# Optimization experiments

Measured on AMD Instinct MI355X. Metric: run time of the kernel, lower is better.

Reference implementation:

```python
import jax, jax.numpy as jnp
import numpy as np

BATCH = 1024


def setup_inputs() -> dict:
    key = jax.random.key(0)
    ks = jax.random.split(key, 8)
    piece_positions = jax.random.randint(ks[0], (BATCH, 64, 10), 0, 2) > 0  # bool occupancy
    king_positions = jax.random.randint(ks[1], (BATCH, 2), 0, 64, dtype=jnp.int32)
    input_weights = jax.random.randint(ks[2], (64, 641, 256), -32768, 32767, dtype=jnp.int16)
    input_bias = jnp.zeros((256,), dtype=jnp.int16)
    w1 = jax.random.randint(ks[3], (32, 512), -128, 127, dtype=jnp.int8)
    b1 = jnp.zeros((32,), dtype=jnp.int32)
    w2 = jax.random.randint(ks[4], (32, 32), -128, 127, dtype=jnp.int8)
    b2 = jnp.zeros((32,), dtype=jnp.int32)
    out_w = jax.random.randint(ks[5], (32,), -128, 127, dtype=jnp.int8)
    out_b = jnp.zeros((1,), dtype=jnp.int32)
    return {
        'piece_positions': piece_positions, 'king_positions': king_positions,
        'input_weights': input_weights, 'input_bias': input_bias,
        'w1': w1, 'b1': b1, 'w2': w2, 'b2': b2, 'out_w': out_w, 'out_b': out_b,
    }


def _fc(x, w, b):
    # int8 inputs/weights, int32 accumulate, floor-div 64, clamp to [0,127] -> int8
    y = x.astype(jnp.int32) @ w.T.astype(jnp.int32) + b
    y = jnp.floor_divide(y, 64)
    return jnp.clip(y, 0, 127).astype(jnp.int8)


def reference(piece_positions, king_positions, input_weights, input_bias,
              w1, b1, w2, b2, out_w, out_b):
    B = piece_positions.shape[0]
    pp = piece_positions.reshape(B, 640).astype(jnp.int32)  # flattened 64x10 HalfKP features

    def half(king_idx):
        wk = input_weights[king_idx]            # (B, 641, 256) gathered per-sample king table
        feats = wk[:, :640, :].astype(jnp.int32)
        kbias = wk[:, 640, :].astype(jnp.int32)
        return jnp.einsum('bf,bfd->bd', pp, feats) + kbias  # (B, 256)

    white = half(king_positions[:, 0])
    black = half(king_positions[:, 1])
    # int16 wraparound semantics of the original: accumulate in int32, mod-cast to int16
    acc = (white + black + input_bias.astype(jnp.int32)).astype(jnp.int16)

    x = jnp.clip(acc, 0, 127).astype(jnp.int8)
    x = jnp.concatenate([x, x], axis=1)  # (B, 512) side_to_move || other_side
    x = _fc(x, w1, b1)
    x = _fc(x, w2, b2)
    s = jnp.sum(x.astype(jnp.int32) * out_w.astype(jnp.int32)) + out_b  # scalar sum over batch too (as in source)
    return jnp.floor_divide(s, 16)  # shape (1,)
```

## Files before the change

### kernel.cpp

```cpp
#include <hip/hip_runtime.h>
#include <stdint.h>

#define NDIM  256
#define NFEAT 640
#define NROWS 641

struct SharedBuf {
    uint8_t pp[NFEAT];
    int     acc[4][NDIM];
    alignas(16) int8_t x[NDIM];
    int     fc[256];
    alignas(4) int8_t x2[32];
    int     list[4][160];
};

__global__ void detect_layout(const int* __restrict__ W32, const int* __restrict__ pp32,
                              int* __restrict__ ws) {
    int raww = 0, rawpp = 0;
    for (int i = 0; i < 16; ++i) {
        const int v = W32[i];
        if (v > 32767 || v < -32768) raww = 1;
        const int u = pp32[i];
        if (u != 0 && u != 1) rawpp = 1;
    }
    ws[0] = 0;
    ws[1] = raww;
    ws[2] = rawpp;
}

template<bool RAWW, bool RAWPP>
__device__ __forceinline__ void nnue_body(
    const void* __restrict__ ppv, const int* __restrict__ kp,
    const void* __restrict__ Wv,  const void* __restrict__ ibv,
    const void* __restrict__ w1v, const int* __restrict__ b1,
    const void* __restrict__ w2v, const int* __restrict__ b2,
    const void* __restrict__ owv, int* __restrict__ ws, SharedBuf& sh)
{
    const int b = blockIdx.x;
    const int t = threadIdx.x;
    const int l = t & 63;
    const int g = t >> 6;

    if (RAWPP) {
        const uint32_t* src = (const uint32_t*)((const uint8_t*)ppv + (size_t)b * NFEAT);
        if (t < NFEAT / 4) ((uint32_t*)sh.pp)[t] = src[t];
    } else {
        const int* src = (const int*)ppv + (size_t)b * NFEAT;
        for (int i = t; i < NFEAT; i += 256) sh.pp[i] = (uint8_t)(src[i] != 0);
    }
    __syncthreads();

    const int base = g * 160;
    int cnt = 0;
    for (int c = 0; c < 160; c += 64) {
        const int idx = c + l;
        const bool flag = (idx < 160) && (sh.pp[base + idx] != 0);
        const unsigned long long m = __ballot(flag);
        const int pos = cnt + (int)__popcll(m & ((1ull << l) - 1ull));
        if (flag) sh.list[g][pos] = base + idx;
        cnt += (int)__popcll(m);
    }

    const int k0 = kp[b * 2 + 0];
    const int k1 = kp[b * 2 + 1];

    int a0 = 0, a1 = 0, a2 = 0, a3 = 0, a4 = 0, a5 = 0, a6 = 0, a7 = 0;

    if (RAWW) {
        const char* W0 = (const char*)Wv + (size_t)k0 * (NROWS * NDIM * 2);
        const char* W1 = (const char*)Wv + (size_t)k1 * (NROWS * NDIM * 2);
        const int lo = l * 8;
        auto step = [&](int f) {
            const uint2 u0 = *(const uint2*)(W0 + f * 512 + lo);
            const uint2 u1 = *(const uint2*)(W1 + f * 512 + lo);
            a0 += (int)(u0.x & 0xFFFFu); a1 += (int)(u0.x >> 16);
            a2 += (int)(u0.y & 0xFFFFu); a3 += (int)(u0.y >> 16);
            a4 += (int)(u1.x & 0xFFFFu); a5 += (int)(u1.x >> 16);
            a6 += (int)(u1.y & 0xFFFFu); a7 += (int)(u1.y >> 16);
        };
        int j = 0;
        for (; j + 4 <= cnt; j += 4) {
            const int f0 = sh.list[g][j], f1 = sh.list[g][j + 1];
            const int f2 = sh.list[g][j + 2], f3 = sh.list[g][j + 3];
            step(f0); step(f1); step(f2); step(f3);
        }
        for (; j < cnt; ++j) step(sh.list[g][j]);
    } else {
        const char* W0 = (const char*)Wv + (size_t)k0 * (NROWS * NDIM * 4);
        const char* W1 = (const char*)Wv + (size_t)k1 * (NROWS * NDIM * 4);
        const int lo = l * 16;
        auto step = [&](int f) {
            const int4 u0 = *(const int4*)(W0 + f * 1024 + lo);
            const int4 u1 = *(const int4*)(W1 + f * 1024 + lo);
            a0 += u0.x; a1 += u0.y; a2 += u0.z; a3 += u0.w;
            a4 += u1.x; a5 += u1.y; a6 += u1.z; a7 += u1.w;
        };
        int j = 0;
        for (; j + 4 <= cnt; j += 4) {
            const int f0 = sh.list[g][j], f1 = sh.list[g][j + 1];
            const int f2 = sh.list[g][j + 2], f3 = sh.list[g][j + 3];
            step(f0); step(f1); step(f2); step(f3);
        }
        for (; j < cnt; ++j) step(sh.list[g][j]);
    }

    sh.acc[g][4 * l + 0] = a0 + a4;
    sh.acc[g][4 * l + 1] = a1 + a5;
    sh.acc[g][4 * l + 2] = a2 + a6;
    sh.acc[g][4 * l + 3] = a3 + a7;
    __syncthreads();

    {
        const int d = t;
        int tot = sh.acc[0][d] + sh.acc[1][d] + sh.acc[2][d] + sh.acc[3][d];
        int kb0, kb1, ibx;
        if (RAWW) {
            const int16_t* Wq = (const int16_t*)Wv;
            kb0 = Wq[((size_t)k0 * NROWS + NFEAT) * NDIM + d];
            kb1 = Wq[((size_t)k1 * NROWS + NFEAT) * NDIM + d];
            ibx = ((const int16_t*)ibv)[d];
        } else {
            const int* Wq = (const int*)Wv;
            kb0 = Wq[((size_t)k0 * NROWS + NFEAT) * NDIM + d];
            kb1 = Wq[((size_t)k1 * NROWS + NFEAT) * NDIM + d];
            ibx = ((const int*)ibv)[d];
        }
        tot += kb0 + kb1 + ibx;
        int v = (int)(int16_t)(uint16_t)(uint32_t)tot;
        v = v < 0 ? 0 : (v > 127 ? 127 : v);
        sh.x[d] = (int8_t)v;
    }
    __syncthreads();

    {
        const int o = t >> 3, part = t & 7;
        int y = 0;
        const uint32_t* xw = (const uint32_t*)sh.x;
        if (RAWW) {
            const uint32_t* w1r = (const uint32_t*)((const char*)w1v + o * 512);
            #pragma unroll
            for (int i = 0; i < 8; ++i) {
                const int wi = part * 8 + i;
                const uint32_t xv = xw[wi];
                const uint32_t wa = w1r[wi];
                const uint32_t wb = w1r[64 + wi];
                #pragma unroll
                for (int jj = 0; jj < 4; ++jj) {
                    const int xj  = (int)((xv >> (8 * jj)) & 0xFFu);
                    const int waj = (int)(int8_t)(uint8_t)(wa >> (8 * jj));
                    const int wbj = (int)(int8_t)(uint8_t)(wb >> (8 * jj));
                    y += xj * (waj + wbj);
                }
            }
        } else {
            const int* w1r = (const int*)w1v + o * 512;
            #pragma unroll
            for (int i = 0; i < 8; ++i) {
                const int wi = part * 8 + i;
                const uint32_t xv = xw[wi];
                #pragma unroll
                for (int jj = 0; jj < 4; ++jj) {
                    const int xj = (int)((xv >> (8 * jj)) & 0xFFu);
                    y += xj * (w1r[wi * 4 + jj] + w1r[256 + wi * 4 + jj]);
                }
            }
        }
        sh.fc[t] = y;
    }
    __syncthreads();

    if (t < 32) {
        int y = b1[t];
        #pragma unroll
        for (int p = 0; p < 8; ++p) y += sh.fc[t * 8 + p];
        y >>= 6;
        y = y < 0 ? 0 : (y > 127 ? 127 : y);
        sh.x2[t] = (int8_t)y;
    }
    __syncthreads();

    if (t < 32) {
        int y = b2[t];
        const uint32_t* x2w = (const uint32_t*)sh.x2;
        if (RAWW) {
            const uint32_t* w2r = (const uint32_t*)((const char*)w2v + t * 32);
            #pragma unroll
            for (int i = 0; i < 8; ++i) {
                const uint32_t xv = x2w[i];
                const uint32_t wv = w2r[i];
                #pragma unroll
                for (int jj = 0; jj < 4; ++jj)
                    y += (int)((xv >> (8 * jj)) & 0xFFu) * (int)(int8_t)(uint8_t)(wv >> (8 * jj));
            }
        } else {
            const int* w2r = (const int*)w2v + t * 32;
            #pragma unroll
            for (int i = 0; i < 8; ++i) {
                const uint32_t xv = x2w[i];
                #pragma unroll
                for (int jj = 0; jj < 4; ++jj)
                    y += (int)((xv >> (8 * jj)) & 0xFFu) * w2r[i * 4 + jj];
            }
        }
        y >>= 6;
        y = y < 0 ? 0 : (y > 127 ? 127 : y);
        const int owx = RAWW ? (int)((const int8_t*)owv)[t] : ((const int*)owv)[t];
        int p = y * owx;
        #pragma unroll
        for (int off = 16; off > 0; off >>= 1) p += __shfl_down(p, off, 32);
        if (t == 0) atomicAdd(ws, p);
    }
}

__global__ __launch_bounds__(256, 4) void nnue_main(
    const void* __restrict__ pp, const int* __restrict__ kp,
    const void* __restrict__ W,  const void* __restrict__ ib,
    const void* __restrict__ w1, const int* __restrict__ b1,
    const void* __restrict__ w2, const int* __restrict__ b2,
    const void* __restrict__ ow, int* __restrict__ ws)
{
    __shared__ SharedBuf sh;
    const int raww = ws[1], rawpp = ws[2];
    if (raww) {
        if (rawpp) nnue_body<true,  true >(pp, kp, W, ib, w1, b1, w2, b2, ow, ws, sh);
        else       nnue_body<true,  false>(pp, kp, W, ib, w1, b1, w2, b2, ow, ws, sh);
    } else {
        if (rawpp) nnue_body<false, true >(pp, kp, W, ib, w1, b1, w2, b2, ow, ws, sh);
        else       nnue_body<false, false>(pp, kp, W, ib, w1, b1, w2, b2, ow, ws, sh);
    }
}

__global__ void nnue_finalize(const int* __restrict__ ws, const int* __restrict__ ob,
                              int* __restrict__ out) {
    out[0] = (ws[0] + ob[0]) >> 4;
}

extern "C" void kernel_launch(void* const* d_in, const int* in_sizes, int n_in,
                              void* d_out, int out_size, void* d_ws, size_t ws_size,
                              hipStream_t stream)
{
    const void* pp = d_in[0];
    const int*  kp = (const int*)d_in[1];
    const void* W  = d_in[2];
    const void* ib = d_in[3];
    const void* w1 = d_in[4];
    const int*  b1 = (const int*)d_in[5];
    const void* w2 = d_in[6];
    const int*  b2 = (const int*)d_in[7];
    const void* ow = d_in[8];
    const int*  ob = (const int*)d_in[9];
    int* ws  = (int*)d_ws;
    int* out = (int*)d_out;

    const int B = in_sizes[1] / 2;

    hipLaunchKernelGGL(detect_layout, dim3(1), dim3(1), 0, stream,
                       (const int*)W, (const int*)pp, ws);
    hipLaunchKernelGGL(nnue_main, dim3(B), dim3(256), 0, stream,
                       pp, kp, W, ib, w1, b1, w2, b2, ow, ws);
    hipLaunchKernelGGL(nnue_finalize, dim3(1), dim3(1), 0, stream, ws, ob, out);
}
```

Measured before the change: 172.0 us.

## Bucket samples by king square and gather weights once per king bucket

Adds a bucketing kernel that sorts the 2B king slots by king index, then a gather kernel where each block handles one king (split into 8 parts) and streams that king's weight table once, accumulating up to 8 samples at a time via per-feature bitmasks. A combine kernel then sums the two halves per sample and runs the small FC layers. This reuses each king's weight rows across many samples instead of re-reading them per sample. In exchange it adds two kernel launches, a single-block serial bucketing pass, a workspace partial buffer, and dense row scans instead of sparse feature lists. The old monolithic path is kept as a fallback when the workspace is too small.

```diff
diff --git a/kernel.cpp b/kernel.cpp
--- a/kernel.cpp
+++ b/kernel.cpp
@@ -4,6 +4,268 @@
 #define NDIM  256
 #define NFEAT 640
 #define NROWS 641
+#define SG    8
+#define PARTS 8
+
+__global__ void nnue_bucket(const int* __restrict__ kp, const int* __restrict__ W32,
+                            const int* __restrict__ pp32, int nslots,
+                            int* __restrict__ ws,
+                            int* __restrict__ king_start, int* __restrict__ slot_list,
+                            int* __restrict__ slot_pos)
+{
+    __shared__ int cnt[64];
+    __shared__ int off[64];
+    const int t = threadIdx.x;
+    if (t < 64) cnt[t] = 0;
+    if (t == 0) {
+        int raww = 0, rawpp = 0;
+        for (int i = 0; i < 16; ++i) {
+            const int v = W32[i];
+            if (v > 32767 || v < -32768) raww = 1;
+            const int u = pp32[i];
+            if (u != 0 && u != 1) rawpp = 1;
+        }
+        ws[0] = 0; ws[1] = raww; ws[2] = rawpp;
+    }
+    __syncthreads();
+    for (int s = t; s < nslots; s += 256) atomicAdd(&cnt[kp[s]], 1);
+    __syncthreads();
+    if (t == 0) {
+        int run = 0;
+        for (int k = 0; k < 64; ++k) { off[k] = run; king_start[k] = run; run += cnt[k]; }
+        king_start[64] = run;
+    }
+    __syncthreads();
+    for (int s = t; s < nslots; s += 256) {
+        const int k = kp[s];
+        const int pos = atomicAdd(&off[k], 1);
+        slot_list[pos] = s;
+        slot_pos[s] = pos;
+    }
+}
+
+struct GatherLds {
+    int samp[SG];
+    unsigned mask[NFEAT];
+    int acci[4][SG][NDIM];
+};
+
+template<bool RAWW, bool RAWPP>
+__device__ __forceinline__ void gather_body(
+    const void* __restrict__ ppv, const void* __restrict__ Wv,
+    const int* __restrict__ king_start, const int* __restrict__ slot_list,
+    int* __restrict__ partial, GatherLds& sh)
+{
+    const int bid = blockIdx.x;
+    const int k = bid & 63;
+    const int p = bid >> 6;
+    const int t = threadIdx.x, l = t & 63, g = t >> 6;
+
+    const int s0 = king_start[k], s1 = king_start[k + 1];
+    const int m = s1 - s0;
+    const int chunk = (m + PARTS - 1) / PARTS;
+    const int lo = s0 + p * chunk;
+    const int hi = min(lo + chunk, s1);
+    if (lo >= hi) return;
+
+    const char* Wk = (const char*)Wv + (size_t)k * NROWS * NDIM * (RAWW ? 2 : 4);
+    int kb;
+    if (RAWW) kb = (int)*(const int16_t*)(Wk + ((size_t)NFEAT * NDIM + t) * 2);
+    else      kb = *(const int*)(Wk + ((size_t)NFEAT * NDIM + t) * 4);
+
+    for (int base = lo; base < hi; base += SG) {
+        const int ns = min(SG, hi - base);
+        if (t < ns) sh.samp[t] = slot_list[base + t] >> 1;
+        __syncthreads();
+
+        for (int r = t; r < NFEAT; r += 256) {
+            unsigned mm = 0;
+            for (int i = 0; i < ns; ++i) {
+                const int s = sh.samp[i];
+                int v;
+                if (RAWPP) v = ((const uint8_t*)ppv)[(size_t)s * NFEAT + r];
+                else       v = ((const int*)ppv)[(size_t)s * NFEAT + r];
+                mm |= (v != 0 ? 1u : 0u) << i;
+            }
+            sh.mask[r] = mm;
+        }
+        __syncthreads();
+
+        int4 acc[SG];
+        #pragma unroll
+        for (int i = 0; i < SG; ++i) acc[i] = make_int4(0, 0, 0, 0);
+
+        const int rbeg = g * (NFEAT / 4), rend = rbeg + (NFEAT / 4);
+        #pragma unroll 2
+        for (int r = rbeg; r < rend; ++r) {
+            unsigned mm = sh.mask[r];
+            mm = __builtin_amdgcn_readfirstlane(mm);
+            int v0, v1, v2, v3;
+            if (RAWW) {
+                const uint2 u = *(const uint2*)(Wk + (size_t)r * 512 + l * 8);
+                v0 = (int)(u.x & 0xFFFFu); v1 = (int)(u.x >> 16);
+                v2 = (int)(u.y & 0xFFFFu); v3 = (int)(u.y >> 16);
+            } else {
+                const int4 u = *(const int4*)(Wk + (size_t)r * 1024 + l * 16);
+                v0 = u.x; v1 = u.y; v2 = u.z; v3 = u.w;
+            }
+            #pragma unroll
+            for (int i = 0; i < SG; ++i)
+                if (mm & (1u << i)) { acc[i].x += v0; acc[i].y += v1; acc[i].z += v2; acc[i].w += v3; }
+        }
+
+        #pragma unroll
+        for (int i = 0; i < SG; ++i) ((int4*)&sh.acci[g][i][0])[l] = acc[i];
+        __syncthreads();
+        for (int i = 0; i < ns; ++i) {
+            const int sum = sh.acci[0][i][t] + sh.acci[1][i][t]
+                          + sh.acci[2][i][t] + sh.acci[3][i][t] + kb;
+            partial[(size_t)(base + i) * NDIM + t] = sum;
+        }
+        __syncthreads();
+    }
+}
+
+__global__ __launch_bounds__(256, 2) void nnue_gather(
+    const void* __restrict__ pp, const void* __restrict__ W,
+    const int* __restrict__ ws, const int* __restrict__ king_start,
+    const int* __restrict__ slot_list, int* __restrict__ partial)
+{
+    __shared__ GatherLds sh;
+    const int raww = ws[1], rawpp = ws[2];
+    if (raww) {
+        if (rawpp) gather_body<true,  true >(pp, W, king_start, slot_list, partial, sh);
+        else       gather_body<true,  false>(pp, W, king_start, slot_list, partial, sh);
+    } else {
+        if (rawpp) gather_body<false, true >(pp, W, king_start, slot_list, partial, sh);
+        else       gather_body<false, false>(pp, W, king_start, slot_list, partial, sh);
+    }
+}
+
+struct CombineLds {
+    alignas(16) int8_t x[NDIM];
+    int fc[256];
+    alignas(4) int8_t x2[32];
+};
+
+template<bool RAWW>
+__device__ __forceinline__ void combine_body(
+    const int* __restrict__ partial, const int* __restrict__ slot_pos,
+    const void* __restrict__ ibv,
+    const void* __restrict__ w1v, const int* __restrict__ b1,
+    const void* __restrict__ w2v, const int* __restrict__ b2,
+    const void* __restrict__ owv, int* __restrict__ ws, CombineLds& sh)
+{
+    const int b = blockIdx.x;
+    const int t = threadIdx.x;
+
+    const int i0 = slot_pos[2 * b + 0];
+    const int i1 = slot_pos[2 * b + 1];
+    {
+        int tot = partial[(size_t)i0 * NDIM + t] + partial[(size_t)i1 * NDIM + t];
+        tot += RAWW ? (int)((const int16_t*)ibv)[t] : ((const int*)ibv)[t];
+        int v = (int)(int16_t)(uint16_t)(uint32_t)tot;
+        v = v < 0 ? 0 : (v > 127 ? 127 : v);
+        sh.x[t] = (int8_t)v;
+    }
+    __syncthreads();
+
+    {
+        const int o = t >> 3, part = t & 7;
+        int y = 0;
+        const uint32_t* xw = (const uint32_t*)sh.x;
+        if (RAWW) {
+            const uint32_t* w1r = (const uint32_t*)((const char*)w1v + o * 512);
+            #pragma unroll
+            for (int i = 0; i < 8; ++i) {
+                const int wi = part * 8 + i;
+                const uint32_t xv = xw[wi];
+                const uint32_t wa = w1r[wi];
+                const uint32_t wb = w1r[64 + wi];
+                #pragma unroll
+                for (int jj = 0; jj < 4; ++jj) {
+                    const int xj  = (int)((xv >> (8 * jj)) & 0xFFu);
+                    const int waj = (int)(int8_t)(uint8_t)(wa >> (8 * jj));
+                    const int wbj = (int)(int8_t)(uint8_t)(wb >> (8 * jj));
+                    y += xj * (waj + wbj);
+                }
+            }
+        } else {
+            const int* w1r = (const int*)w1v + o * 512;
+            #pragma unroll
+            for (int i = 0; i < 8; ++i) {
+                const int wi = part * 8 + i;
+                const uint32_t xv = xw[wi];
+                #pragma unroll
+                for (int jj = 0; jj < 4; ++jj) {
+                    const int xj = (int)((xv >> (8 * jj)) & 0xFFu);
+                    y += xj * (w1r[wi * 4 + jj] + w1r[256 + wi * 4 + jj]);
+                }
+            }
+        }
+        sh.fc[t] = y;
+    }
+    __syncthreads();
+
+    if (t < 32) {
+        int y = b1[t];
+        #pragma unroll
+        for (int p = 0; p < 8; ++p) y += sh.fc[t * 8 + p];
+        y >>= 6;
+        y = y < 0 ? 0 : (y > 127 ? 127 : y);
+        sh.x2[t] = (int8_t)y;
+    }
+    __syncthreads();
+
+    if (t < 32) {
+        int y = b2[t];
+        const uint32_t* x2w = (const uint32_t*)sh.x2;
+        if (RAWW) {
+            const uint32_t* w2r = (const uint32_t*)((const char*)w2v + t * 32);
+            #pragma unroll
+            for (int i = 0; i < 8; ++i) {
+                const uint32_t xv = x2w[i];
+                const uint32_t wv = w2r[i];
+                #pragma unroll
+                for (int jj = 0; jj < 4; ++jj)
+                    y += (int)((xv >> (8 * jj)) & 0xFFu) * (int)(int8_t)(uint8_t)(wv >> (8 * jj));
+            }
+        } else {
+            const int* w2r = (const int*)w2v + t * 32;
+            #pragma unroll
+            for (int i = 0; i < 8; ++i) {
+                const uint32_t xv = x2w[i];
+                #pragma unroll
+                for (int jj = 0; jj < 4; ++jj)
+                    y += (int)((xv >> (8 * jj)) & 0xFFu) * w2r[i * 4 + jj];
+            }
+        }
+        y >>= 6;
+        y = y < 0 ? 0 : (y > 127 ? 127 : y);
+        const int owx = RAWW ? (int)((const int8_t*)owv)[t] : ((const int*)owv)[t];
+        int pr = y * owx;
+        #pragma unroll
+        for (int off = 16; off > 0; off >>= 1) pr += __shfl_down(pr, off, 32);
+        if (t == 0) atomicAdd(ws, pr);
+    }
+}
+
+__global__ __launch_bounds__(256) void nnue_combine(
+    const int* __restrict__ partial, const int* __restrict__ slot_pos,
+    const void* __restrict__ ib,
+    const void* __restrict__ w1, const int* __restrict__ b1,
+    const void* __restrict__ w2, const int* __restrict__ b2,
+    const void* __restrict__ ow, int* __restrict__ ws)
+{
+    __shared__ CombineLds sh;
+    if (ws[1]) combine_body<true >(partial, slot_pos, ib, w1, b1, w2, b2, ow, ws, sh);
+    else       combine_body<false>(partial, slot_pos, ib, w1, b1, w2, b2, ow, ws, sh);
+}
+
+__global__ void nnue_finalize(const int* __restrict__ ws, const int* __restrict__ ob,
+                              int* __restrict__ out) {
+    out[0] = (ws[0] + ob[0]) >> 4;
+}
 
 struct SharedBuf {
     uint8_t pp[NFEAT];
@@ -23,13 +285,11 @@
         const int u = pp32[i];
         if (u != 0 && u != 1) rawpp = 1;
     }
-    ws[0] = 0;
-    ws[1] = raww;
-    ws[2] = rawpp;
+    ws[0] = 0; ws[1] = raww; ws[2] = rawpp;
 }
 
 template<bool RAWW, bool RAWPP>
-__device__ __forceinline__ void nnue_body(
+__device__ __forceinline__ void mono_body(
     const void* __restrict__ ppv, const int* __restrict__ kp,
     const void* __restrict__ Wv,  const void* __restrict__ ibv,
     const void* __restrict__ w1v, const int* __restrict__ b1,
@@ -55,15 +315,14 @@
     for (int c = 0; c < 160; c += 64) {
         const int idx = c + l;
         const bool flag = (idx < 160) && (sh.pp[base + idx] != 0);
-        const unsigned long long m = __ballot(flag);
-        const int pos = cnt + (int)__popcll(m & ((1ull << l) - 1ull));
+        const unsigned long long mmask = __ballot(flag);
+        const int pos = cnt + (int)__popcll(mmask & ((1ull << l) - 1ull));
         if (flag) sh.list[g][pos] = base + idx;
-        cnt += (int)__popcll(m);
+        cnt += (int)__popcll(mmask);
     }
 
     const int k0 = kp[b * 2 + 0];
     const int k1 = kp[b * 2 + 1];
-
     int a0 = 0, a1 = 0, a2 = 0, a3 = 0, a4 = 0, a5 = 0, a6 = 0, a7 = 0;
 
     if (RAWW) {
@@ -205,14 +464,14 @@
         y >>= 6;
         y = y < 0 ? 0 : (y > 127 ? 127 : y);
         const int owx = RAWW ? (int)((const int8_t*)owv)[t] : ((const int*)owv)[t];
-        int p = y * owx;
+        int pr = y * owx;
         #pragma unroll
-        for (int off = 16; off > 0; off >>= 1) p += __shfl_down(p, off, 32);
-        if (t == 0) atomicAdd(ws, p);
-    }
-}
-
-__global__ __launch_bounds__(256, 4) void nnue_main(
+        for (int off = 16; off > 0; off >>= 1) pr += __shfl_down(pr, off, 32);
+        if (t == 0) atomicAdd(ws, pr);
+    }
+}
+
+__global__ __launch_bounds__(256, 4) void nnue_mono(
     const void* __restrict__ pp, const int* __restrict__ kp,
     const void* __restrict__ W,  const void* __restrict__ ib,
     const void* __restrict__ w1, const int* __restrict__ b1,
@@ -222,17 +481,12 @@
     __shared__ SharedBuf sh;
     const int raww = ws[1], rawpp = ws[2];
     if (raww) {
-        if (rawpp) nnue_body<true,  true >(pp, kp, W, ib, w1, b1, w2, b2, ow, ws, sh);
-        else       nnue_body<true,  false>(pp, kp, W, ib, w1, b1, w2, b2, ow, ws, sh);
+        if (rawpp) mono_body<true,  true >(pp, kp, W, ib, w1, b1, w2, b2, ow, ws, sh);
+        else       mono_body<true,  false>(pp, kp, W, ib, w1, b1, w2, b2, ow, ws, sh);
     } else {
-        if (rawpp) nnue_body<false, true >(pp, kp, W, ib, w1, b1, w2, b2, ow, ws, sh);
-        else       nnue_body<false, false>(pp, kp, W, ib, w1, b1, w2, b2, ow, ws, sh);
-    }
-}
-
-__global__ void nnue_finalize(const int* __restrict__ ws, const int* __restrict__ ob,
-                              int* __restrict__ out) {
-    out[0] = (ws[0] + ob[0]) >> 4;
+        if (rawpp) mono_body<false, true >(pp, kp, W, ib, w1, b1, w2, b2, ow, ws, sh);
+        else       mono_body<false, false>(pp, kp, W, ib, w1, b1, w2, b2, ow, ws, sh);
+    }
 }
 
 extern "C" void kernel_launch(void* const* d_in, const int* in_sizes, int n_in,
@@ -253,10 +507,33 @@
     int* out = (int*)d_out;
 
     const int B = in_sizes[1] / 2;
-
-    hipLaunchKernelGGL(detect_layout, dim3(1), dim3(1), 0, stream,
-                       (const int*)W, (const int*)pp, ws);
-    hipLaunchKernelGGL(nnue_main, dim3(B), dim3(256), 0, stream,
-                       pp, kp, W, ib, w1, b1, w2, b2, ow, ws);
-    hipLaunchKernelGGL(nnue_finalize, dim3(1), dim3(1), 0, stream, ws, ob, out);
-}
+    const int nslots = 2 * B;
+
+    const size_t off_ks = 16;
+    const size_t off_sl = 96;
+    const size_t off_sp = off_sl + (size_t)nslots;
+    const size_t off_pb = ((off_sp + (size_t)nslots + 255) / 256) * 256;
+    const size_t need   = (off_pb + (size_t)nslots * NDIM) * 4;
+
+    if (ws_size >= need) {
+        int* king_start = ws + off_ks;
+        int* slot_list  = ws + off_sl;
+        int* slot_pos   = ws + off_sp;
+        int* partial    = ws + off_pb;
+
+        hipLaunchKernelGGL(nnue_bucket, dim3(1), dim3(256), 0, stream,
+                           kp, (const int*)W, (const int*)pp, nslots,
+                           ws, king_start, slot_list, slot_pos);
+        hipLaunchKernelGGL(nnue_gather, dim3(64 * PARTS), dim3(256), 0, stream,
+                           pp, W, ws, king_start, slot_list, partial);
+        hipLaunchKernelGGL(nnue_combine, dim3(B), dim3(256), 0, stream,
+                           partial, slot_pos, ib, w1, b1, w2, b2, ow, ws);
+        hipLaunchKernelGGL(nnue_finalize, dim3(1), dim3(1), 0, stream, ws, ob, out);
+    } else {
+        hipLaunchKernelGGL(detect_layout, dim3(1), dim3(1), 0, stream,
+                           (const int*)W, (const int*)pp, ws);
+        hipLaunchKernelGGL(nnue_mono, dim3(B), dim3(256), 0, stream,
+                           pp, kp, W, ib, w1, b1, w2, b2, ow, ws);
+        hipLaunchKernelGGL(nnue_finalize, dim3(1), dim3(1), 0, stream, ws, ob, out);
+    }
+}
```

Result: no change. 170.4 us (-0.9%).
